# Kernel optimization log

Measured on AMD Instinct MI355X. Metric: run time of the kernel, lower is better.

Reference implementation:

```python
import jax, jax.numpy as jnp
import numpy as np

N_SRC = 50000
N_DST = 50000
E = 800000
D = 128
OUT = 128


def setup_inputs() -> dict:
    key = jax.random.key(0)
    k1, k2, k3, k4, k5, k6 = jax.random.split(key, 6)
    lim = 1.0 / np.sqrt(D)
    return {
        "x_src": jax.random.normal(k1, (N_SRC, D), dtype=jnp.float32),
        "x_dst": jax.random.normal(k2, (N_DST, D), dtype=jnp.float32),
        "edge_src": jax.random.randint(k3, (E,), 0, N_SRC, dtype=jnp.int64),
        "edge_dst": jax.random.randint(k4, (E,), 0, N_DST, dtype=jnp.int64),
        "num_dst": N_DST,
        # learned params (torch nn.Linear: y = x @ W.T + b), stored here as [in, out]
        "W_neigh": jax.random.uniform(k5, (D, OUT), jnp.float32, -lim, lim),
        "b_neigh": jnp.zeros((OUT,), jnp.float32),
        "W_self": jax.random.uniform(k6, (D, OUT), jnp.float32, -lim, lim),
        "b_self": jnp.zeros((OUT,), jnp.float32),
    }


def reference(x_src, x_dst, edge_src, edge_dst, num_dst, W_neigh, b_neigh, W_self, b_self):
    # gather source features per edge: [E, D]
    neigh_feats = x_src[edge_src]
    # scatter-mean onto destination nodes
    summed = jax.ops.segment_sum(neigh_feats, edge_dst, num_segments=num_dst)  # [num_dst, D]
    count = jax.ops.segment_sum(jnp.ones((edge_dst.shape[0], 1), x_src.dtype), edge_dst,
                                num_segments=num_dst)
    agg = summed / jnp.clip(count, 1.0)
    # dual linear + add
    return agg @ W_neigh + b_neigh + x_dst @ W_self + b_self
```

## Files before the change

### kernel.cpp

```cpp
#include <hip/hip_runtime.h>

#define D 128
#define TM 64
#define CBITS 7
#define CSIZE 128
#define MAXNB 512
#define CAPB 2560

typedef __attribute__((ext_vector_type(8))) short bf16x8;
typedef __attribute__((ext_vector_type(4))) float f32x4;


__device__ __forceinline__ unsigned short f32_to_bf16(float x) {
    unsigned u = __float_as_uint(x);
    u += 0x7FFFu + ((u >> 16) & 1u);
    return (unsigned short)(u >> 16);
}
__device__ __forceinline__ float bf16_to_f32(unsigned short h) {
    return __uint_as_float(((unsigned)h) << 16);
}

__global__ __launch_bounds__(256) void prep_kernel(
    const float* __restrict__ Wn, const float* __restrict__ Ws,
    unsigned short* __restrict__ Wtn, unsigned short* __restrict__ Wts,
    int* __restrict__ gcursor, int NB) {
    const int stride = gridDim.x * 256;
    for (int i = blockIdx.x * 256 + threadIdx.x; i < D * D; i += stride) {
        int n = i >> 7, k = i & (D - 1);
        Wtn[i] = f32_to_bf16(Wn[k * D + n]);
        Wts[i] = f32_to_bf16(Ws[k * D + n]);
    }
    for (int i = blockIdx.x * 256 + threadIdx.x; i < NB; i += stride)
        gcursor[i] = 0;
}

__global__ __launch_bounds__(256) void fused_part_gemm_kernel(
    const int* __restrict__ edge_src, const int* __restrict__ edge_dst,
    int* __restrict__ gcursor, int* __restrict__ packed, int E, int NB,
    const float* __restrict__ x_src, const float* __restrict__ x_dst,
    const unsigned short* __restrict__ Wtn, const unsigned short* __restrict__ Wts,
    const float* __restrict__ bn, const float* __restrict__ bs,
    unsigned short* __restrict__ y16, float* __restrict__ out,
    int M_SRC, int N, int nblk, int blkA, int pstride) {
    __shared__ __align__(16) char smem[TM * 136 * 2];
    const int t = threadIdx.x;
    const int idx = (int)blockIdx.x;

    const bool isPart = (idx % pstride == 0) && (idx / pstride < nblk);

    if (isPart) {
        const int pid = idx / pstride;
        int* lh    = (int*)smem;
        int* lbase = lh + MAXNB;
        for (int i = t; i < NB; i += 256) lh[i] = 0;
        __syncthreads();
        const int base = pid * 2048;
        int es[8], ed[8];
        #pragma unroll
        for (int i = 0; i < 8; ++i) {
            int e = base + t + i * 256;
            if (e < E) { es[i] = edge_src[e]; ed[i] = edge_dst[e]; }
            else ed[i] = -1;
        }
        #pragma unroll
        for (int i = 0; i < 8; ++i)
            if (ed[i] >= 0) atomicAdd(&lh[ed[i] >> CBITS], 1);
        __syncthreads();
        for (int i = t; i < NB; i += 256) {
            int v = lh[i];
            lbase[i] = v ? atomicAdd(&gcursor[i], v) : 0;
        }
        __syncthreads();
        for (int i = t; i < NB; i += 256) lh[i] = 0;
        __syncthreads();
        #pragma unroll
        for (int i = 0; i < 8; ++i) {
            if (ed[i] >= 0) {
                int bk = ed[i] >> CBITS;
                int pos = lbase[bk] + atomicAdd(&lh[bk], 1);
                if (pos < CAPB)
                    packed[(size_t)bk * CAPB + pos] =
                        (es[i] << CBITS) | (ed[i] & (CSIZE - 1));
            }
        }
        return;
    }

    typedef unsigned short ushort136[136];
    ushort136* LA = (ushort136*)smem;

    const int npb  = min((idx + pstride - 1) / pstride, nblk);
    const int gb   = idx - npb;
    const bool isA  = gb < blkA;
    const int  row0 = (isA ? gb : gb - blkA) * TM;
    const int  M    = isA ? M_SRC : N;
    const float* Ap = isA ? x_src : x_dst;
    const unsigned short* Wp = isA ? Wtn : Wts;

    {
        const float4* Av = (const float4*)Ap;
        #pragma unroll
        for (int i = 0; i < 8; ++i) {
            int vi = t + i * 256;
            int r = vi >> 5, c4 = vi & 31;
            int sr = min(row0 + r, M - 1);
            float4 v = Av[(size_t)sr * 32 + c4];
            ushort4 p;
            p.x = f32_to_bf16(v.x); p.y = f32_to_bf16(v.y);
            p.z = f32_to_bf16(v.z); p.w = f32_to_bf16(v.w);
            *(ushort4*)&LA[r][c4 * 4] = p;
        }
    }
    __syncthreads();

    const int lane = t & 63;
    const int wv   = t >> 6;
    const int wr   = wv & 1;
    const int wc   = wv >> 1;
    const int lr   = lane & 15;
    const int g    = lane >> 4;

    f32x4 acc[2][4];
    #pragma unroll
    for (int i = 0; i < 2; ++i)
        #pragma unroll
        for (int j = 0; j < 4; ++j) acc[i][j] = (f32x4){0.f, 0.f, 0.f, 0.f};

    #pragma unroll
    for (int kt = 0; kt < 4; ++kt) {
        const int kk = kt * 32 + g * 8;
        bf16x8 b0 = *(const bf16x8*)&Wp[(size_t)(wc * 64 + 0 * 16 + lr) * D + kk];
        bf16x8 b1 = *(const bf16x8*)&Wp[(size_t)(wc * 64 + 1 * 16 + lr) * D + kk];
        bf16x8 b2 = *(const bf16x8*)&Wp[(size_t)(wc * 64 + 2 * 16 + lr) * D + kk];
        bf16x8 b3 = *(const bf16x8*)&Wp[(size_t)(wc * 64 + 3 * 16 + lr) * D + kk];
        bf16x8 a0 = *(const bf16x8*)&LA[wr * 32 + lr][kk];
        bf16x8 a1 = *(const bf16x8*)&LA[wr * 32 + 16 + lr][kk];
        acc[0][0] = __builtin_amdgcn_mfma_f32_16x16x32_bf16(a0, b0, acc[0][0], 0, 0, 0);
        acc[0][1] = __builtin_amdgcn_mfma_f32_16x16x32_bf16(a0, b1, acc[0][1], 0, 0, 0);
        acc[0][2] = __builtin_amdgcn_mfma_f32_16x16x32_bf16(a0, b2, acc[0][2], 0, 0, 0);
        acc[0][3] = __builtin_amdgcn_mfma_f32_16x16x32_bf16(a0, b3, acc[0][3], 0, 0, 0);
        acc[1][0] = __builtin_amdgcn_mfma_f32_16x16x32_bf16(a1, b0, acc[1][0], 0, 0, 0);
        acc[1][1] = __builtin_amdgcn_mfma_f32_16x16x32_bf16(a1, b1, acc[1][1], 0, 0, 0);
        acc[1][2] = __builtin_amdgcn_mfma_f32_16x16x32_bf16(a1, b2, acc[1][2], 0, 0, 0);
        acc[1][3] = __builtin_amdgcn_mfma_f32_16x16x32_bf16(a1, b3, acc[1][3], 0, 0, 0);
    }

    if (isA) {
        #pragma unroll
        for (int i = 0; i < 2; ++i) {
            #pragma unroll
            for (int j = 0; j < 4; ++j) {
                int col = wc * 64 + j * 16 + lr;
                #pragma unroll
                for (int r = 0; r < 4; ++r) {
                    int row = row0 + wr * 32 + i * 16 + g * 4 + r;
                    if (row < M)
                        y16[(size_t)row * D + col] = f32_to_bf16(acc[i][j][r]);
                }
            }
        }
    } else {
        #pragma unroll
        for (int i = 0; i < 2; ++i) {
            #pragma unroll
            for (int j = 0; j < 4; ++j) {
                int col = wc * 64 + j * 16 + lr;
                float bias = bn[col] + bs[col];
                #pragma unroll
                for (int r = 0; r < 4; ++r) {
                    int row = row0 + wr * 32 + i * 16 + g * 4 + r;
                    if (row < M)
                        out[(size_t)row * D + col] = acc[i][j][r] + bias;
                }
            }
        }
    }
}

__global__ __launch_bounds__(256) void fine_kernel(
    const int* __restrict__ packed, const int* __restrict__ gcursor,
    int* __restrict__ off_beg, int* __restrict__ off_end,
    int* __restrict__ eidx, int N) {
    __shared__ int dcount[4][CSIZE];
    __shared__ int wbase[4][CSIZE];
    __shared__ int sbuf[CSIZE];
    const int b  = blockIdx.x;
    const int d0 = b << CBITS;
    const int beg = b * CAPB;
    const int cnt = min(gcursor[b], CAPB);
    const int t = threadIdx.x;
    const int wv = t >> 6;

    if (t < CSIZE) {
        dcount[0][t] = 0; dcount[1][t] = 0;
        dcount[2][t] = 0; dcount[3][t] = 0;
    }
    __syncthreads();
    for (int i = t; i < cnt; i += 256)
        atomicAdd(&dcount[wv][packed[beg + i] & (CSIZE - 1)], 1);
    __syncthreads();
    int tot = 0;
    if (t < CSIZE) {
        tot = dcount[0][t] + dcount[1][t] + dcount[2][t] + dcount[3][t];
        sbuf[t] = tot;
    }
    __syncthreads();
    for (int ofs = 1; ofs < CSIZE; ofs <<= 1) {
        int u = (t < CSIZE && t >= ofs) ? sbuf[t - ofs] : 0;
        __syncthreads();
        if (t < CSIZE) sbuf[t] += u;
        __syncthreads();
    }
    if (t < CSIZE) {
        int excl = sbuf[t] - tot;
        int d = d0 + t;
        if (d < N) {
            off_beg[d] = beg + excl;
            off_end[d] = beg + excl + tot;
        }
        int run = excl;
        #pragma unroll
        for (int w = 0; w < 4; ++w) {
            wbase[w][t] = run;
            run += dcount[w][t];
        }
    }
    __syncthreads();
    for (int i = t; i < cnt; i += 256) {
        int p = packed[beg + i];
        int pos = beg + atomicAdd(&wbase[wv][p & (CSIZE - 1)], 1);
        eidx[pos] = p >> CBITS;
    }
}

__global__ __launch_bounds__(256) void gather_out_kernel(
    const unsigned short* __restrict__ y16,
    const int* __restrict__ off_beg,
    const int* __restrict__ off_end,
    const int* __restrict__ eidx,
    float* __restrict__ out, int N) {
    const int wave = (int)(((long long)blockIdx.x * blockDim.x + threadIdx.x) >> 6);
    const int lane = threadIdx.x & 63;
    if (wave >= N) return;
    const int h = lane >> 4;
    const int c = lane & 15;
    const int beg = off_beg[wave];
    const int end = off_end[wave];

    float acc[8];
    #pragma unroll
    for (int j = 0; j < 8; ++j) acc[j] = 0.f;

    for (int i = beg + h; i < end; i += 4) {
        int s = eidx[i];
        const int4 v = *reinterpret_cast<const int4*>(y16 + (size_t)s * D + c * 8);
        const unsigned short* hs = (const unsigned short*)&v;
        #pragma unroll
        for (int j = 0; j < 8; ++j) acc[j] += bf16_to_f32(hs[j]);
    }

    #pragma unroll
    for (int j = 0; j < 8; ++j) {
        acc[j] += __shfl_down(acc[j], 32);
        acc[j] += __shfl_down(acc[j], 16);
    }

    if (h == 0) {
        const float inv = 1.0f / fmaxf((float)(end - beg), 1.0f);
        float4* o = reinterpret_cast<float4*>(out + (size_t)wave * D) + c * 2;
        float4 c0 = o[0], c1 = o[1];
        c0.x = fmaf(acc[0], inv, c0.x);
        c0.y = fmaf(acc[1], inv, c0.y);
        c0.z = fmaf(acc[2], inv, c0.z);
        c0.w = fmaf(acc[3], inv, c0.w);
        c1.x = fmaf(acc[4], inv, c1.x);
        c1.y = fmaf(acc[5], inv, c1.y);
        c1.z = fmaf(acc[6], inv, c1.z);
        c1.w = fmaf(acc[7], inv, c1.w);
        o[0] = c0;
        o[1] = c1;
    }
}

extern "C" void kernel_launch(void* const* d_in, const int* in_sizes, int n_in,
                              void* d_out, int out_size, void* d_ws, size_t ws_size,
                              hipStream_t stream) {
    const float* x_src    = (const float*)d_in[0];
    const float* x_dst    = (const float*)d_in[1];
    const int*   edge_src = (const int*)d_in[2];
    const int*   edge_dst = (const int*)d_in[3];
    const float* Wn = (const float*)d_in[5];
    const float* bn = (const float*)d_in[6];
    const float* Ws = (const float*)d_in[7];
    const float* bs = (const float*)d_in[8];

    const int E     = in_sizes[2];
    const int N     = in_sizes[1] / D;
    const int M_SRC = in_sizes[0] / D;

    const int NB   = (N + CSIZE - 1) >> CBITS;
    const int nblk = (E + 2047) / 2048;

    unsigned short* y16 = (unsigned short*)d_ws;
    unsigned short* Wtn = y16 + (size_t)M_SRC * D;
    unsigned short* Wts = Wtn + D * D;
    int* packed  = (int*)(Wts + D * D);
    int* eidx    = packed + (size_t)NB * CAPB;
    int* off_beg = eidx + (size_t)NB * CAPB;
    int* off_end = off_beg + N;
    int* gcursor = off_end + N;

    const int T = 256;
    prep_kernel<<<32, T, 0, stream>>>(Wn, Ws, Wtn, Wts, gcursor, NB);

    const int blkA = (M_SRC + TM - 1) / TM;
    const int blkB = (N + TM - 1) / TM;
    const int total = nblk + blkA + blkB;
    const int pstride = total / nblk > 1 ? total / nblk : 1;
    fused_part_gemm_kernel<<<total, T, 0, stream>>>(
        edge_src, edge_dst, gcursor, packed, E, NB,
        x_src, x_dst, Wtn, Wts, bn, bs, y16, (float*)d_out,
        M_SRC, N, nblk, blkA, pstride);

    fine_kernel<<<NB, T, 0, stream>>>(packed, gcursor, off_beg, off_end, eidx, N);

    gather_out_kernel<<<(N + 3) / 4, T, 0, stream>>>(
        y16, off_beg, off_end, eidx, (float*)d_out, N);
}
```

Before: 81.71 us.

## Stage weights in LDS, widen fine_kernel to 512 threads, unroll gather by two

The GEMM blocks now copy the full bf16 weight matrix into shared memory and read the MFMA B operands from LDS instead of global memory. LDS use per block grows to about 52KB, which may reduce occupancy. fine_kernel runs with 512 threads and eight per-wave histograms to bin each bucket faster. The gather loop processes two edges per iteration to raise memory-level parallelism.

```diff
diff --git a/kernel.cpp b/kernel.cpp
--- a/kernel.cpp
+++ b/kernel.cpp
@@ -42,7 +42,7 @@
     const float* __restrict__ bn, const float* __restrict__ bs,
     unsigned short* __restrict__ y16, float* __restrict__ out,
     int M_SRC, int N, int nblk, int blkA, int pstride) {
-    __shared__ __align__(16) char smem[TM * 136 * 2];
+    __shared__ __align__(16) char smem[TM * 136 * 2 + D * 136 * 2];
     const int t = threadIdx.x;
     const int idx = (int)blockIdx.x;
 
@@ -88,6 +88,7 @@
 
     typedef unsigned short ushort136[136];
     ushort136* LA = (ushort136*)smem;
+    ushort136* LW = (ushort136*)(smem + TM * 136 * 2);
 
     const int npb  = min((idx + pstride - 1) / pstride, nblk);
     const int gb   = idx - npb;
@@ -110,6 +111,13 @@
             p.z = f32_to_bf16(v.z); p.w = f32_to_bf16(v.w);
             *(ushort4*)&LA[r][c4 * 4] = p;
         }
+        const int4* Wv = (const int4*)Wp;
+        #pragma unroll
+        for (int i = 0; i < 8; ++i) {
+            int vi = t + i * 256;
+            int r = vi >> 4, c8 = vi & 15;
+            *(int4*)&LW[r][c8 * 8] = Wv[vi];
+        }
     }
     __syncthreads();
 
@@ -128,13 +136,12 @@
 
     #pragma unroll
     for (int kt = 0; kt < 4; ++kt) {
-        const int kk = kt * 32 + g * 8;
-        bf16x8 b0 = *(const bf16x8*)&Wp[(size_t)(wc * 64 + 0 * 16 + lr) * D + kk];
-        bf16x8 b1 = *(const bf16x8*)&Wp[(size_t)(wc * 64 + 1 * 16 + lr) * D + kk];
-        bf16x8 b2 = *(const bf16x8*)&Wp[(size_t)(wc * 64 + 2 * 16 + lr) * D + kk];
-        bf16x8 b3 = *(const bf16x8*)&Wp[(size_t)(wc * 64 + 3 * 16 + lr) * D + kk];
-        bf16x8 a0 = *(const bf16x8*)&LA[wr * 32 + lr][kk];
-        bf16x8 a1 = *(const bf16x8*)&LA[wr * 32 + 16 + lr][kk];
+        bf16x8 b0 = *(const bf16x8*)&LW[wc * 64 + 0 * 16 + lr][kt * 32 + g * 8];
+        bf16x8 b1 = *(const bf16x8*)&LW[wc * 64 + 1 * 16 + lr][kt * 32 + g * 8];
+        bf16x8 b2 = *(const bf16x8*)&LW[wc * 64 + 2 * 16 + lr][kt * 32 + g * 8];
+        bf16x8 b3 = *(const bf16x8*)&LW[wc * 64 + 3 * 16 + lr][kt * 32 + g * 8];
+        bf16x8 a0 = *(const bf16x8*)&LA[wr * 32 + lr][kt * 32 + g * 8];
+        bf16x8 a1 = *(const bf16x8*)&LA[wr * 32 + 16 + lr][kt * 32 + g * 8];
         acc[0][0] = __builtin_amdgcn_mfma_f32_16x16x32_bf16(a0, b0, acc[0][0], 0, 0, 0);
         acc[0][1] = __builtin_amdgcn_mfma_f32_16x16x32_bf16(a0, b1, acc[0][1], 0, 0, 0);
         acc[0][2] = __builtin_amdgcn_mfma_f32_16x16x32_bf16(a0, b2, acc[0][2], 0, 0, 0);
@@ -177,12 +184,12 @@
     }
 }
 
-__global__ __launch_bounds__(256) void fine_kernel(
+__global__ __launch_bounds__(512) void fine_kernel(
     const int* __restrict__ packed, const int* __restrict__ gcursor,
     int* __restrict__ off_beg, int* __restrict__ off_end,
     int* __restrict__ eidx, int N) {
-    __shared__ int dcount[4][CSIZE];
-    __shared__ int wbase[4][CSIZE];
+    __shared__ int dcount[8][CSIZE];
+    __shared__ int wbase[8][CSIZE];
     __shared__ int sbuf[CSIZE];
     const int b  = blockIdx.x;
     const int d0 = b << CBITS;
@@ -192,16 +199,17 @@
     const int wv = t >> 6;
 
     if (t < CSIZE) {
-        dcount[0][t] = 0; dcount[1][t] = 0;
-        dcount[2][t] = 0; dcount[3][t] = 0;
-    }
-    __syncthreads();
-    for (int i = t; i < cnt; i += 256)
+        #pragma unroll
+        for (int w = 0; w < 8; ++w) dcount[w][t] = 0;
+    }
+    __syncthreads();
+    for (int i = t; i < cnt; i += 512)
         atomicAdd(&dcount[wv][packed[beg + i] & (CSIZE - 1)], 1);
     __syncthreads();
     int tot = 0;
     if (t < CSIZE) {
-        tot = dcount[0][t] + dcount[1][t] + dcount[2][t] + dcount[3][t];
+        #pragma unroll
+        for (int w = 0; w < 8; ++w) tot += dcount[w][t];
         sbuf[t] = tot;
     }
     __syncthreads();
@@ -220,13 +228,13 @@
         }
         int run = excl;
         #pragma unroll
-        for (int w = 0; w < 4; ++w) {
+        for (int w = 0; w < 8; ++w) {
             wbase[w][t] = run;
             run += dcount[w][t];
         }
     }
     __syncthreads();
-    for (int i = t; i < cnt; i += 256) {
+    for (int i = t; i < cnt; i += 512) {
         int p = packed[beg + i];
         int pos = beg + atomicAdd(&wbase[wv][p & (CSIZE - 1)], 1);
         eidx[pos] = p >> CBITS;
@@ -251,7 +259,19 @@
     #pragma unroll
     for (int j = 0; j < 8; ++j) acc[j] = 0.f;
 
-    for (int i = beg + h; i < end; i += 4) {
+    int i = beg + h;
+    for (; i + 4 < end; i += 8) {
+        int s0 = eidx[i];
+        int s1 = eidx[i + 4];
+        const int4 v0 = *reinterpret_cast<const int4*>(y16 + (size_t)s0 * D + c * 8);
+        const int4 v1 = *reinterpret_cast<const int4*>(y16 + (size_t)s1 * D + c * 8);
+        const unsigned short* h0 = (const unsigned short*)&v0;
+        const unsigned short* h1 = (const unsigned short*)&v1;
+        #pragma unroll
+        for (int j = 0; j < 8; ++j)
+            acc[j] += bf16_to_f32(h0[j]) + bf16_to_f32(h1[j]);
+    }
+    if (i < end) {
         int s = eidx[i];
         const int4 v = *reinterpret_cast<const int4*>(y16 + (size_t)s * D + c * 8);
         const unsigned short* hs = (const unsigned short*)&v;
@@ -322,7 +342,7 @@
         x_src, x_dst, Wtn, Wts, bn, bs, y16, (float*)d_out,
         M_SRC, N, nblk, blkA, pstride);
 
-    fine_kernel<<<NB, T, 0, stream>>>(packed, gcursor, off_beg, off_end, eidx, N);
+    fine_kernel<<<NB, 512, 0, stream>>>(packed, gcursor, off_beg, off_end, eidx, N);
 
     gather_out_kernel<<<(N + 3) / 4, T, 0, stream>>>(
         y16, off_beg, off_end, eidx, (float*)d_out, N);
```

After: 73.84 us. -9.6%, faster.
